# Performance work log

Hardware: AMD Instinct MI355X
Metric: run time of the kernel (lower is better)

## Reference

```python
import jax, jax.numpy as jnp
import numpy as np

B, NPER, K, H = 256, 512, 8, 16  # events, particles/event, knn k, hidden_dim
N = B * NPER


def _edge_conv(h, Wc, bc):
    """DynamicEdgeConv: per-event kNN graph, edge MLP on [x_i, x_j-x_i], max-aggregate."""
    d = h.shape[-1]
    hb = h.reshape(B, NPER, d)
    sq = jnp.sum(hb * hb, axis=-1)                                   # [B,n]
    d2 = sq[:, :, None] + sq[:, None, :] - 2.0 * jnp.einsum('bnd,bmd->bnm', hb, hb)
    _, idx = jax.lax.top_k(-d2, K)                                   # [B,n,K] nearest (incl. self)
    xj = jax.vmap(lambda hh, ii: hh[ii])(hb, idx)                    # [B,n,K,d] gather
    xi = jnp.broadcast_to(hb[:, :, None, :], xj.shape)               # [B,n,K,d]
    e = jnp.concatenate([xi, xj - xi], axis=-1)                      # [B,n,K,2d]
    m = jax.nn.elu(e @ Wc + bc)                                      # [B,n,K,H]
    return jnp.max(m, axis=2).reshape(N, -1)                         # scatter-max over neighbors


def setup_inputs() -> dict:
    key = jax.random.key(0)
    ks = jax.random.split(key, 10)
    def lin(k, fin, fout):
        return jax.random.normal(k, (fin, fout), jnp.float32) / np.sqrt(fin)
    x_pf = jax.random.normal(ks[0], (N, 4), jnp.float32)
    batch_pf = jnp.repeat(jnp.arange(B, dtype=jnp.int64), NPER)
    return {
        'x_pf': x_pf, 'batch_pf': batch_pf,
        'W1': lin(ks[1], 4, H),  'b1': jnp.zeros((H,), jnp.float32),
        'W2': lin(ks[2], H, H),  'b2': jnp.zeros((H,), jnp.float32),
        'Wc': lin(ks[3], 2 * H, H), 'bc': jnp.zeros((H,), jnp.float32),
        'Wo1': lin(ks[4], H, 8), 'bo1': jnp.zeros((8,), jnp.float32),
        'Wo2': lin(ks[5], 8, 4), 'bo2': jnp.zeros((4,), jnp.float32),
        'Wo3': lin(ks[6], 4, 1), 'bo3': jnp.zeros((1,), jnp.float32),
    }


def reference(x_pf, batch_pf, W1, b1, W2, b2, Wc, bc, Wo1, bo1, Wo2, bo2, Wo3, bo3):
    # pf_encode: Linear-ELU-Linear-ELU (assumes contiguous equal-size events per batch_pf)
    h = jax.nn.elu(x_pf @ W1 + b1)
    h = jax.nn.elu(h @ W2 + b2)                                      # [N,H]
    # two DynamicEdgeConv passes with SHARED weights (same self.conv called twice)
    f1 = _edge_conv(h, Wc, bc)
    f2 = _edge_conv(f1, Wc, bc)
    # avg_pool_x with cluster == batch -> per-event mean
    pooled = f2.reshape(B, NPER, -1).mean(axis=1)                    # [B,H]
    o = jax.nn.elu(pooled @ Wo1 + bo1)
    o = jax.nn.elu(o @ Wo2 + bo2)
    out = o @ Wo3 + bo3                                              # [B,1]
    return out, jnp.arange(B)
```

## Files before the change

### kernel.cpp

```cpp
#include <hip/hip_runtime.h>

#define NEV 256
#define NP  512
#define HD  16
#define GPAD 20
#define KBS 36

typedef short s16x8  __attribute__((ext_vector_type(8)));
typedef float f32x16 __attribute__((ext_vector_type(16)));

#define Z16 {0.f,0.f,0.f,0.f,0.f,0.f,0.f,0.f,0.f,0.f,0.f,0.f,0.f,0.f,0.f,0.f}

__device__ __forceinline__ float elu_f(float x) {
    return x > 0.0f ? x : (__expf(x) - 1.0f);
}
__device__ __forceinline__ unsigned umin_(unsigned a, unsigned b) { return a < b ? a : b; }
__device__ __forceinline__ unsigned med3u(unsigned a, unsigned b, unsigned c) {
    unsigned d;
    asm("v_med3_u32 %0, %1, %2, %3" : "=v"(d) : "v"(a), "v"(b), "v"(c));
    return d;
}
__device__ __forceinline__ unsigned short rneb(float f) {
    unsigned u = __float_as_uint(f);
    return (unsigned short)((u + 0x7FFFu + ((u >> 16) & 1u)) >> 16);
}
__device__ __forceinline__ float bits2f(unsigned short b) {
    return __uint_as_float(((unsigned)b) << 16);
}

__global__ __launch_bounds__(512) void suep_fused(
    const float* __restrict__ x_pf,
    const float* __restrict__ W1,  const float* __restrict__ b1,
    const float* __restrict__ W2,  const float* __restrict__ b2,
    const float* __restrict__ Wc,  const float* __restrict__ bc,
    const float* __restrict__ Wo1, const float* __restrict__ bo1,
    const float* __restrict__ Wo2, const float* __restrict__ bo2,
    const float* __restrict__ Wo3, const float* __restrict__ bo3,
    float* __restrict__ out)
{
    __shared__ unsigned kb[NP * KBS];
    __shared__ s16x8 fragH[16][64];
    __shared__ s16x8 fragL[16][64];
    __shared__ float sSq[NP];
    __shared__ float sW1[64],  sB1[HD];
    __shared__ float sW2[256], sB2[HD];
    __shared__ float sWcB[256], sWcD[256], sBc[HD];
    __shared__ float sWo1[128], sBo1[8], sWo2[32], sBo2[4], sWo3[4], sBo3[1];
    __shared__ float sRedM[8];
    __shared__ float sRed[8][HD];
    __shared__ float sPool[HD];

    const int tid   = threadIdx.x;
    const int ev    = blockIdx.x;
    const int l     = tid & 63;
    const int w     = tid >> 6;
    const int c32   = l & 31;
    const int khalf = l >> 5;

    if (tid < 64) sW1[tid] = W1[tid];
    if (tid < HD) { sB1[tid] = b1[tid]; sB2[tid] = b2[tid]; sBc[tid] = bc[tid]; }
    if (tid < 256) {
        sW2[tid] = W2[tid];
        float wb = Wc[256 + tid];
        sWcB[tid] = wb;
        sWcD[tid] = Wc[tid] - wb;
    }
    if (tid < 128) sWo1[tid] = Wo1[tid];
    if (tid < 8)   sBo1[tid] = bo1[tid];
    if (tid < 32)  sWo2[tid] = Wo2[tid];
    if (tid < 4)   { sBo2[tid] = bo2[tid]; sWo3[tid] = Wo3[tid]; }
    if (tid == 0)  sBo3[0] = bo3[0];
    __syncthreads();

    float4 xv = ((const float4*)x_pf)[ev * NP + tid];
    float e1[HD];
#pragma unroll
    for (int c = 0; c < HD; ++c) {
        float a = sB1[c];
        a = fmaf(xv.x, sW1[0 * HD + c], a);
        a = fmaf(xv.y, sW1[1 * HD + c], a);
        a = fmaf(xv.z, sW1[2 * HD + c], a);
        a = fmaf(xv.w, sW1[3 * HD + c], a);
        e1[c] = elu_f(a);
    }
    float h[HD];
#pragma unroll
    for (int c = 0; c < HD; ++c) {
        float a = sB2[c];
#pragma unroll
        for (int f = 0; f < HD; ++f) a = fmaf(e1[f], sW2[f * HD + c], a);
        h[c] = elu_f(a);
    }

    auto build_frags = [&](const float* hr) -> float {
        s16x8 vh0, vh1, vl0, vl1;
        float sq = 0.0f;
#pragma unroll
        for (int k = 0; k < HD; ++k) {
            unsigned short hb = rneb(hr[k]);
            float fh = bits2f(hb);
            float rr = hr[k] - fh;
            unsigned short lb = rneb(rr);
            float fl = bits2f(lb);
            float ht = fh + fl;
            sq = fmaf(ht, ht, sq);
            if (k < 8) { vh0[k] = (short)hb; vl0[k] = (short)lb; }
            else       { vh1[k - 8] = (short)hb; vl1[k - 8] = (short)lb; }
        }
        int b = tid >> 5, r = tid & 31;
        fragH[b][r]      = vh0;
        fragH[b][r + 32] = vh1;
        fragL[b][r]      = vl0;
        fragL[b][r + 32] = vl1;
        sSq[tid] = sq;
        float m = sq;
#pragma unroll
        for (int d = 32; d >= 1; d >>= 1) m = fmaxf(m, __shfl_xor(m, d, 64));
        if (l == 0) sRedM[w] = m;
        __syncthreads();
        float mx = sRedM[0];
#pragma unroll
        for (int i = 1; i < 8; ++i) mx = fmaxf(mx, sRedM[i]);
        return mx + 1.0f;
    };

    auto do_conv = [&](const float* hr, float* fout) {
        float Cv = build_frags(hr);

        s16x8 Ah0 = fragH[2 * w][l],     Al0 = fragL[2 * w][l];
        s16x8 Ah1 = fragH[2 * w + 1][l], Al1 = fragL[2 * w + 1][l];

        unsigned t0 = ~0u, t1 = ~0u, t2 = ~0u, t3 = ~0u,
                 t4 = ~0u, t5 = ~0u, t6 = ~0u, t7 = ~0u;
#define INS(KEY) do { unsigned kk = (KEY);            \
        t7 = med3u(t6, kk, t7); t6 = med3u(t5, kk, t6); \
        t5 = med3u(t4, kk, t5); t4 = med3u(t3, kk, t4); \
        t3 = med3u(t2, kk, t3); t2 = med3u(t1, kk, t2); \
        t1 = med3u(t0, kk, t1); t0 = umin_(kk, t0); } while (0)

        auto cs = [&](int s, f32x16& a0, f32x16& a1) {
            s16x8 Bh = fragH[s][l], Bl = fragL[s][l];
            f32x16 z = Z16;
            a0 = __builtin_amdgcn_mfma_f32_32x32x16_bf16(Al0, Bh, z,  0, 0, 0);
            a0 = __builtin_amdgcn_mfma_f32_32x32x16_bf16(Ah0, Bl, a0, 0, 0, 0);
            a0 = __builtin_amdgcn_mfma_f32_32x32x16_bf16(Ah0, Bh, a0, 0, 0, 0);
            a1 = __builtin_amdgcn_mfma_f32_32x32x16_bf16(Al1, Bh, z,  0, 0, 0);
            a1 = __builtin_amdgcn_mfma_f32_32x32x16_bf16(Ah1, Bl, a1, 0, 0, 0);
            a1 = __builtin_amdgcn_mfma_f32_32x32x16_bf16(Ah1, Bh, a1, 0, 0, 0);
        };

        unsigned* wp = &kb[(64 * w + 4 * khalf) * KBS + c32];
        auto st = [&](int s, const f32x16& a0, const f32x16& a1) {
            float base = Cv + sSq[s * 32 + c32];
            unsigned colb = (unsigned)(s * 32 + c32);
#pragma unroll
            for (int q = 0; q < 16; ++q) {
                const int roff = (q & 3) + 8 * (q >> 2);
                wp[roff * KBS] =
                    (__float_as_uint(fmaf(-2.0f, a0[q], base)) & 0xFFFFFE00u) | colb;
                wp[(32 + roff) * KBS] =
                    (__float_as_uint(fmaf(-2.0f, a1[q], base)) & 0xFFFFFE00u) | colb;
            }
        };

        const uint4* rp = (const uint4*)&kb[tid * KBS];
        auto scan = [&]() {
#pragma unroll
            for (int g = 0; g < 8; ++g) {
                uint4 k4 = rp[g];
                INS(k4.x); INS(k4.y); INS(k4.z); INS(k4.w);
            }
        };

        f32x16 aA, aB, nA, nB;
        cs(0, aA, aB);
        for (int s = 0; s < 16; s += 2) {
            st(s, aA, aB);
            cs(s + 1, nA, nB);
            asm volatile("s_waitcnt lgkmcnt(0)" ::: "memory");
            scan();
            st(s + 1, nA, nB);
            if (s + 2 < 16) cs(s + 2, aA, aB);
            asm volatile("s_waitcnt lgkmcnt(0)" ::: "memory");
            scan();
        }
#undef INS

        float gg[HD], bb[HD];
#pragma unroll
        for (int c = 0; c < HD; ++c) { gg[c] = 0.0f; bb[c] = sBc[c]; }
#pragma unroll
        for (int f = 0; f < HD; ++f) {
            float hf = hr[f];
#pragma unroll
            for (int c = 0; c < HD; ++c) {
                gg[c] = fmaf(hf, sWcB[f * HD + c], gg[c]);
                bb[c] = fmaf(hf, sWcD[f * HD + c], bb[c]);
            }
        }
        __syncthreads();
        float (*sG)[GPAD] = reinterpret_cast<float(*)[GPAD]>(kb);
        ((float4*)(&sG[tid][0]))[0] = make_float4(gg[0], gg[1], gg[2], gg[3]);
        ((float4*)(&sG[tid][0]))[1] = make_float4(gg[4], gg[5], gg[6], gg[7]);
        ((float4*)(&sG[tid][0]))[2] = make_float4(gg[8], gg[9], gg[10], gg[11]);
        ((float4*)(&sG[tid][0]))[3] = make_float4(gg[12], gg[13], gg[14], gg[15]);
        __syncthreads();

        int idx[8] = { (int)(t0 & 511u), (int)(t1 & 511u), (int)(t2 & 511u),
                       (int)(t3 & 511u), (int)(t4 & 511u), (int)(t5 & 511u),
                       (int)(t6 & 511u), (int)(t7 & 511u) };
        float z[HD];
#pragma unroll
        for (int c = 0; c < HD; ++c) z[c] = -3.4e38f;
#pragma unroll
        for (int n = 0; n < 8; ++n) {
            const float4* r4 = (const float4*)(&sG[idx[n]][0]);
            float4 va = r4[0], vb = r4[1], vc = r4[2], vd = r4[3];
            z[0]  = fmaxf(z[0],  bb[0]  + va.x);
            z[1]  = fmaxf(z[1],  bb[1]  + va.y);
            z[2]  = fmaxf(z[2],  bb[2]  + va.z);
            z[3]  = fmaxf(z[3],  bb[3]  + va.w);
            z[4]  = fmaxf(z[4],  bb[4]  + vb.x);
            z[5]  = fmaxf(z[5],  bb[5]  + vb.y);
            z[6]  = fmaxf(z[6],  bb[6]  + vb.z);
            z[7]  = fmaxf(z[7],  bb[7]  + vb.w);
            z[8]  = fmaxf(z[8],  bb[8]  + vc.x);
            z[9]  = fmaxf(z[9],  bb[9]  + vc.y);
            z[10] = fmaxf(z[10], bb[10] + vc.z);
            z[11] = fmaxf(z[11], bb[11] + vc.w);
            z[12] = fmaxf(z[12], bb[12] + vd.x);
            z[13] = fmaxf(z[13], bb[13] + vd.y);
            z[14] = fmaxf(z[14], bb[14] + vd.z);
            z[15] = fmaxf(z[15], bb[15] + vd.w);
        }
#pragma unroll
        for (int c = 0; c < HD; ++c) fout[c] = elu_f(z[c]);
    };

    float f1[HD], f2[HD];
    do_conv(h, f1);
    do_conv(f1, f2);

#pragma unroll
    for (int m = 32; m >= 1; m >>= 1) {
#pragma unroll
        for (int c = 0; c < HD; ++c) f2[c] += __shfl_xor(f2[c], m, 64);
    }
    if (l == 0) {
        ((float4*)(&sRed[w][0]))[0] = make_float4(f2[0], f2[1], f2[2], f2[3]);
        ((float4*)(&sRed[w][0]))[1] = make_float4(f2[4], f2[5], f2[6], f2[7]);
        ((float4*)(&sRed[w][0]))[2] = make_float4(f2[8], f2[9], f2[10], f2[11]);
        ((float4*)(&sRed[w][0]))[3] = make_float4(f2[12], f2[13], f2[14], f2[15]);
    }
    __syncthreads();
    if (tid < HD) {
        float s = 0.0f;
#pragma unroll
        for (int ww = 0; ww < 8; ++ww) s += sRed[ww][tid];
        sPool[tid] = s * (1.0f / (float)NP);
    }
    __syncthreads();

    if (tid == 0) {
        float o1[8];
#pragma unroll
        for (int c = 0; c < 8; ++c) {
            float a = sBo1[c];
#pragma unroll
            for (int f = 0; f < HD; ++f) a = fmaf(sPool[f], sWo1[f * 8 + c], a);
            o1[c] = elu_f(a);
        }
        float o2[4];
#pragma unroll
        for (int c = 0; c < 4; ++c) {
            float a = sBo2[c];
#pragma unroll
            for (int f = 0; f < 8; ++f) a = fmaf(o1[f], sWo2[f * 4 + c], a);
            o2[c] = elu_f(a);
        }
        float o3 = sBo3[0];
#pragma unroll
        for (int f = 0; f < 4; ++f) o3 = fmaf(o2[f], sWo3[f], o3);
        out[ev] = o3;
        out[NEV + ev] = (float)ev;
    }
}

extern "C" void kernel_launch(void* const* d_in, const int* in_sizes, int n_in,
                              void* d_out, int out_size, void* d_ws, size_t ws_size,
                              hipStream_t stream) {
    const float* x_pf = (const float*)d_in[0];
    const float* W1  = (const float*)d_in[2];
    const float* b1  = (const float*)d_in[3];
    const float* W2  = (const float*)d_in[4];
    const float* b2  = (const float*)d_in[5];
    const float* Wc  = (const float*)d_in[6];
    const float* bc  = (const float*)d_in[7];
    const float* Wo1 = (const float*)d_in[8];
    const float* bo1 = (const float*)d_in[9];
    const float* Wo2 = (const float*)d_in[10];
    const float* bo2 = (const float*)d_in[11];
    const float* Wo3 = (const float*)d_in[12];
    const float* bo3 = (const float*)d_in[13];
    float* out = (float*)d_out;

    hipLaunchKernelGGL(suep_fused, dim3(NEV), dim3(512), 0, stream,
                       x_pf, W1, b1, W2, b2, Wc, bc,
                       Wo1, bo1, Wo2, bo2, Wo3, bo3, out);
}
```

Before: 143.2 us.

## Split per-event work across 1024 threads with half-row kNN scans and merge

Doubles the block to 1024 threads, so each wave handles 32 query rows instead of 64. The two 32-lane halves scan separate halves of each key tile, and their sorted top-8 lists are merged with cross-lane shuffles. Fragment building, the edge-MLP precompute (the gather term in one half and the bias term in the other) and the neighbor max-gather are also split across the two thread halves, with conv outputs passed through shared memory. The aim is more waves per CU, with less per-thread register pressure and serial scan latency. The cost is extra barriers, shuffles and shared-memory round trips.

```diff
diff --git a/kernel.cpp b/kernel.cpp
--- a/kernel.cpp
+++ b/kernel.cpp
@@ -3,7 +3,6 @@
 #define NEV 256
 #define NP  512
 #define HD  16
-#define GPAD 20
 #define KBS 36
 
 typedef short s16x8  __attribute__((ext_vector_type(8)));
@@ -27,8 +26,11 @@
 __device__ __forceinline__ float bits2f(unsigned short b) {
     return __uint_as_float(((unsigned)b) << 16);
 }
-
-__global__ __launch_bounds__(512) void suep_fused(
+__device__ __forceinline__ unsigned sx32(unsigned v) {
+    return (unsigned)__shfl_xor((int)v, 32, 64);
+}
+
+__global__ __launch_bounds__(1024, 4) void suep_fused(
     const float* __restrict__ x_pf,
     const float* __restrict__ W1,  const float* __restrict__ b1,
     const float* __restrict__ W2,  const float* __restrict__ b2,
@@ -42,20 +44,19 @@
     __shared__ s16x8 fragH[16][64];
     __shared__ s16x8 fragL[16][64];
     __shared__ float sSq[NP];
-    __shared__ float sW1[64],  sB1[HD];
-    __shared__ float sW2[256], sB2[HD];
+    __shared__ float sW1[64], sB1[HD], sW2[256], sB2[HD];
     __shared__ float sWcB[256], sWcD[256], sBc[HD];
     __shared__ float sWo1[128], sBo1[8], sWo2[32], sBo2[4], sWo3[4], sBo3[1];
     __shared__ float sRedM[8];
-    __shared__ float sRed[8][HD];
+    __shared__ float sRed[16][HD];
     __shared__ float sPool[HD];
 
-    const int tid   = threadIdx.x;
-    const int ev    = blockIdx.x;
-    const int l     = tid & 63;
-    const int w     = tid >> 6;
-    const int c32   = l & 31;
-    const int khalf = l >> 5;
+    const int tid = threadIdx.x, ev = blockIdx.x;
+    const int l = tid & 63, w = tid >> 6;
+    const int n = tid & 511;
+    const bool loT = (tid < 512);
+    const int c32 = l & 31, kh = l >> 5;
+    const int row = 32 * w + c32;
 
     if (tid < 64) sW1[tid] = W1[tid];
     if (tid < HD) { sB1[tid] = b1[tid]; sB2[tid] = b2[tid]; sBc[tid] = bc[tid]; }
@@ -72,51 +73,53 @@
     if (tid == 0)  sBo3[0] = bo3[0];
     __syncthreads();
 
-    float4 xv = ((const float4*)x_pf)[ev * NP + tid];
-    float e1[HD];
-#pragma unroll
-    for (int c = 0; c < HD; ++c) {
-        float a = sB1[c];
-        a = fmaf(xv.x, sW1[0 * HD + c], a);
-        a = fmaf(xv.y, sW1[1 * HD + c], a);
-        a = fmaf(xv.z, sW1[2 * HD + c], a);
-        a = fmaf(xv.w, sW1[3 * HD + c], a);
-        e1[c] = elu_f(a);
+    float hr[HD];
+    {
+        float4 xv = ((const float4*)x_pf)[ev * NP + n];
+        float e1[HD];
+#pragma unroll
+        for (int c = 0; c < HD; ++c) {
+            float a = sB1[c];
+            a = fmaf(xv.x, sW1[0 * HD + c], a);
+            a = fmaf(xv.y, sW1[1 * HD + c], a);
+            a = fmaf(xv.z, sW1[2 * HD + c], a);
+            a = fmaf(xv.w, sW1[3 * HD + c], a);
+            e1[c] = elu_f(a);
+        }
+#pragma unroll
+        for (int c = 0; c < HD; ++c) {
+            float a = sB2[c];
+#pragma unroll
+            for (int f = 0; f < HD; ++f) a = fmaf(e1[f], sW2[f * HD + c], a);
+            hr[c] = elu_f(a);
+        }
     }
-    float h[HD];
-#pragma unroll
-    for (int c = 0; c < HD; ++c) {
-        float a = sB2[c];
-#pragma unroll
-        for (int f = 0; f < HD; ++f) a = fmaf(e1[f], sW2[f * HD + c], a);
-        h[c] = elu_f(a);
-    }
-
-    auto build_frags = [&](const float* hr) -> float {
-        s16x8 vh0, vh1, vl0, vl1;
+
+    auto build_frags = [&]() -> float {
+        s16x8 v0, v1;
         float sq = 0.0f;
 #pragma unroll
         for (int k = 0; k < HD; ++k) {
             unsigned short hb = rneb(hr[k]);
             float fh = bits2f(hb);
-            float rr = hr[k] - fh;
-            unsigned short lb = rneb(rr);
-            float fl = bits2f(lb);
-            float ht = fh + fl;
-            sq = fmaf(ht, ht, sq);
-            if (k < 8) { vh0[k] = (short)hb; vl0[k] = (short)lb; }
-            else       { vh1[k - 8] = (short)hb; vl1[k - 8] = (short)lb; }
-        }
-        int b = tid >> 5, r = tid & 31;
-        fragH[b][r]      = vh0;
-        fragH[b][r + 32] = vh1;
-        fragL[b][r]      = vl0;
-        fragL[b][r + 32] = vl1;
-        sSq[tid] = sq;
-        float m = sq;
-#pragma unroll
-        for (int d = 32; d >= 1; d >>= 1) m = fmaxf(m, __shfl_xor(m, d, 64));
-        if (l == 0) sRedM[w] = m;
+            unsigned short lb = rneb(hr[k] - fh);
+            if (loT) {
+                float ht = fh + bits2f(lb);
+                sq = fmaf(ht, ht, sq);
+            }
+            unsigned short vb = loT ? hb : lb;
+            if (k < 8) v0[k] = (short)vb; else v1[k - 8] = (short)vb;
+        }
+        s16x8 (*fr)[64] = loT ? fragH : fragL;
+        fr[n >> 5][n & 31]      = v0;
+        fr[n >> 5][(n & 31) + 32] = v1;
+        if (loT) {
+            sSq[n] = sq;
+            float m = sq;
+#pragma unroll
+            for (int d = 32; d >= 1; d >>= 1) m = fmaxf(m, __shfl_xor(m, d, 64));
+            if (l == 0) sRedM[w] = m;
+        }
         __syncthreads();
         float mx = sRedM[0];
 #pragma unroll
@@ -124,142 +127,161 @@
         return mx + 1.0f;
     };
 
-    auto do_conv = [&](const float* hr, float* fout) {
-        float Cv = build_frags(hr);
-
-        s16x8 Ah0 = fragH[2 * w][l],     Al0 = fragL[2 * w][l];
-        s16x8 Ah1 = fragH[2 * w + 1][l], Al1 = fragL[2 * w + 1][l];
+    auto do_conv = [&](bool last) {
+        float Cv = build_frags();
+
+        s16x8 Ah = fragH[w][l], Al = fragL[w][l];
 
         unsigned t0 = ~0u, t1 = ~0u, t2 = ~0u, t3 = ~0u,
                  t4 = ~0u, t5 = ~0u, t6 = ~0u, t7 = ~0u;
-#define INS(KEY) do { unsigned kk = (KEY);            \
+#define INS(KEY) do { unsigned kk = (KEY);              \
         t7 = med3u(t6, kk, t7); t6 = med3u(t5, kk, t6); \
         t5 = med3u(t4, kk, t5); t4 = med3u(t3, kk, t4); \
         t3 = med3u(t2, kk, t3); t2 = med3u(t1, kk, t2); \
         t1 = med3u(t0, kk, t1); t0 = umin_(kk, t0); } while (0)
 
-        auto cs = [&](int s, f32x16& a0, f32x16& a1) {
+        auto cs = [&](int s, f32x16& a) {
             s16x8 Bh = fragH[s][l], Bl = fragL[s][l];
             f32x16 z = Z16;
-            a0 = __builtin_amdgcn_mfma_f32_32x32x16_bf16(Al0, Bh, z,  0, 0, 0);
-            a0 = __builtin_amdgcn_mfma_f32_32x32x16_bf16(Ah0, Bl, a0, 0, 0, 0);
-            a0 = __builtin_amdgcn_mfma_f32_32x32x16_bf16(Ah0, Bh, a0, 0, 0, 0);
-            a1 = __builtin_amdgcn_mfma_f32_32x32x16_bf16(Al1, Bh, z,  0, 0, 0);
-            a1 = __builtin_amdgcn_mfma_f32_32x32x16_bf16(Ah1, Bl, a1, 0, 0, 0);
-            a1 = __builtin_amdgcn_mfma_f32_32x32x16_bf16(Ah1, Bh, a1, 0, 0, 0);
+            a = __builtin_amdgcn_mfma_f32_32x32x16_bf16(Al, Bh, z, 0, 0, 0);
+            a = __builtin_amdgcn_mfma_f32_32x32x16_bf16(Ah, Bl, a, 0, 0, 0);
+            a = __builtin_amdgcn_mfma_f32_32x32x16_bf16(Ah, Bh, a, 0, 0, 0);
         };
 
-        unsigned* wp = &kb[(64 * w + 4 * khalf) * KBS + c32];
-        auto st = [&](int s, const f32x16& a0, const f32x16& a1) {
-            float base = Cv + sSq[s * 32 + c32];
-            unsigned colb = (unsigned)(s * 32 + c32);
+        unsigned* wp = &kb[(32 * w + 4 * kh) * KBS + c32];
+        auto st = [&](int s, const f32x16& a) {
+            float base = Cv + sSq[32 * s + c32];
+            unsigned colb = (unsigned)(32 * s + c32);
 #pragma unroll
             for (int q = 0; q < 16; ++q) {
                 const int roff = (q & 3) + 8 * (q >> 2);
                 wp[roff * KBS] =
-                    (__float_as_uint(fmaf(-2.0f, a0[q], base)) & 0xFFFFFE00u) | colb;
-                wp[(32 + roff) * KBS] =
-                    (__float_as_uint(fmaf(-2.0f, a1[q], base)) & 0xFFFFFE00u) | colb;
+                    (__float_as_uint(fmaf(-2.0f, a[q], base)) & 0xFFFFFE00u) | colb;
             }
         };
 
-        const uint4* rp = (const uint4*)&kb[tid * KBS];
+        const uint4* rp = (const uint4*)&kb[row * KBS + 16 * kh];
         auto scan = [&]() {
 #pragma unroll
-            for (int g = 0; g < 8; ++g) {
+            for (int g = 0; g < 4; ++g) {
                 uint4 k4 = rp[g];
                 INS(k4.x); INS(k4.y); INS(k4.z); INS(k4.w);
             }
         };
 
-        f32x16 aA, aB, nA, nB;
-        cs(0, aA, aB);
+        f32x16 a0, a1;
+        cs(0, a0);
         for (int s = 0; s < 16; s += 2) {
-            st(s, aA, aB);
-            cs(s + 1, nA, nB);
+            st(s, a0);
+            cs(s + 1, a1);
             asm volatile("s_waitcnt lgkmcnt(0)" ::: "memory");
             scan();
-            st(s + 1, nA, nB);
-            if (s + 2 < 16) cs(s + 2, aA, aB);
+            st(s + 1, a1);
+            if (s + 2 < 16) cs(s + 2, a0);
             asm volatile("s_waitcnt lgkmcnt(0)" ::: "memory");
             scan();
         }
 #undef INS
 
-        float gg[HD], bb[HD];
-#pragma unroll
-        for (int c = 0; c < HD; ++c) { gg[c] = 0.0f; bb[c] = sBc[c]; }
-#pragma unroll
-        for (int f = 0; f < HD; ++f) {
-            float hf = hr[f];
-#pragma unroll
-            for (int c = 0; c < HD; ++c) {
-                gg[c] = fmaf(hf, sWcB[f * HD + c], gg[c]);
-                bb[c] = fmaf(hf, sWcD[f * HD + c], bb[c]);
+        unsigned m0 = umin_(t0, sx32(t7)), m1 = umin_(t1, sx32(t6)),
+                 m2 = umin_(t2, sx32(t5)), m3 = umin_(t3, sx32(t4)),
+                 m4 = umin_(t4, sx32(t3)), m5 = umin_(t5, sx32(t2)),
+                 m6 = umin_(t6, sx32(t1)), m7 = umin_(t7, sx32(t0));
+
+        float gb[HD];
+        {
+            const float* Wm = loT ? sWcB : sWcD;
+#pragma unroll
+            for (int c = 0; c < HD; ++c) gb[c] = loT ? 0.0f : sBc[c];
+#pragma unroll
+            for (int f = 0; f < HD; ++f) {
+                float hf = hr[f];
+#pragma unroll
+                for (int c = 0; c < HD; ++c) gb[c] = fmaf(hf, Wm[f * HD + c], gb[c]);
             }
         }
         __syncthreads();
-        float (*sG)[GPAD] = reinterpret_cast<float(*)[GPAD]>(kb);
-        ((float4*)(&sG[tid][0]))[0] = make_float4(gg[0], gg[1], gg[2], gg[3]);
-        ((float4*)(&sG[tid][0]))[1] = make_float4(gg[4], gg[5], gg[6], gg[7]);
-        ((float4*)(&sG[tid][0]))[2] = make_float4(gg[8], gg[9], gg[10], gg[11]);
-        ((float4*)(&sG[tid][0]))[3] = make_float4(gg[12], gg[13], gg[14], gg[15]);
+        float* gr = (float*)&kb[n * KBS + (loT ? 0 : 16)];
+        ((float4*)gr)[0] = make_float4(gb[0], gb[1], gb[2], gb[3]);
+        ((float4*)gr)[1] = make_float4(gb[4], gb[5], gb[6], gb[7]);
+        ((float4*)gr)[2] = make_float4(gb[8], gb[9], gb[10], gb[11]);
+        ((float4*)gr)[3] = make_float4(gb[12], gb[13], gb[14], gb[15]);
         __syncthreads();
 
-        int idx[8] = { (int)(t0 & 511u), (int)(t1 & 511u), (int)(t2 & 511u),
-                       (int)(t3 & 511u), (int)(t4 & 511u), (int)(t5 & 511u),
-                       (int)(t6 & 511u), (int)(t7 & 511u) };
+        int j0 = (int)((kh ? m4 : m0) & 511u), j1 = (int)((kh ? m5 : m1) & 511u);
+        int j2 = (int)((kh ? m6 : m2) & 511u), j3 = (int)((kh ? m7 : m3) & 511u);
         float z[HD];
-#pragma unroll
-        for (int c = 0; c < HD; ++c) z[c] = -3.4e38f;
-#pragma unroll
-        for (int n = 0; n < 8; ++n) {
-            const float4* r4 = (const float4*)(&sG[idx[n]][0]);
-            float4 va = r4[0], vb = r4[1], vc = r4[2], vd = r4[3];
-            z[0]  = fmaxf(z[0],  bb[0]  + va.x);
-            z[1]  = fmaxf(z[1],  bb[1]  + va.y);
-            z[2]  = fmaxf(z[2],  bb[2]  + va.z);
-            z[3]  = fmaxf(z[3],  bb[3]  + va.w);
-            z[4]  = fmaxf(z[4],  bb[4]  + vb.x);
-            z[5]  = fmaxf(z[5],  bb[5]  + vb.y);
-            z[6]  = fmaxf(z[6],  bb[6]  + vb.z);
-            z[7]  = fmaxf(z[7],  bb[7]  + vb.w);
-            z[8]  = fmaxf(z[8],  bb[8]  + vc.x);
-            z[9]  = fmaxf(z[9],  bb[9]  + vc.y);
-            z[10] = fmaxf(z[10], bb[10] + vc.z);
-            z[11] = fmaxf(z[11], bb[11] + vc.w);
-            z[12] = fmaxf(z[12], bb[12] + vd.x);
-            z[13] = fmaxf(z[13], bb[13] + vd.y);
-            z[14] = fmaxf(z[14], bb[14] + vd.z);
-            z[15] = fmaxf(z[15], bb[15] + vd.w);
-        }
-#pragma unroll
-        for (int c = 0; c < HD; ++c) fout[c] = elu_f(z[c]);
+        {
+            const float4* g0 = (const float4*)&kb[j0 * KBS];
+            const float4* g1 = (const float4*)&kb[j1 * KBS];
+            const float4* g2 = (const float4*)&kb[j2 * KBS];
+            const float4* g3 = (const float4*)&kb[j3 * KBS];
+#pragma unroll
+            for (int qq = 0; qq < 4; ++qq) {
+                float4 va = g0[qq], vb = g1[qq], vc = g2[qq], vd = g3[qq];
+                z[4*qq+0] = fmaxf(fmaxf(va.x, vb.x), fmaxf(vc.x, vd.x));
+                z[4*qq+1] = fmaxf(fmaxf(va.y, vb.y), fmaxf(vc.y, vd.y));
+                z[4*qq+2] = fmaxf(fmaxf(va.z, vb.z), fmaxf(vc.z, vd.z));
+                z[4*qq+3] = fmaxf(fmaxf(va.w, vb.w), fmaxf(vc.w, vd.w));
+            }
+        }
+#pragma unroll
+        for (int c = 0; c < HD; ++c) z[c] = fmaxf(z[c], __shfl_xor(z[c], 32, 64));
+
+        float fo[HD];
+        if (kh == 0) {
+            const float4* br = (const float4*)&kb[row * KBS + 16];
+#pragma unroll
+            for (int qq = 0; qq < 4; ++qq) {
+                float4 vb = br[qq];
+                fo[4*qq+0] = elu_f(z[4*qq+0] + vb.x);
+                fo[4*qq+1] = elu_f(z[4*qq+1] + vb.y);
+                fo[4*qq+2] = elu_f(z[4*qq+2] + vb.z);
+                fo[4*qq+3] = elu_f(z[4*qq+3] + vb.w);
+            }
+        }
+
+        if (!last) {
+            __syncthreads();
+            if (kh == 0) {
+                float4* fr = (float4*)&kb[row * KBS];
+                fr[0] = make_float4(fo[0], fo[1], fo[2], fo[3]);
+                fr[1] = make_float4(fo[4], fo[5], fo[6], fo[7]);
+                fr[2] = make_float4(fo[8], fo[9], fo[10], fo[11]);
+                fr[3] = make_float4(fo[12], fo[13], fo[14], fo[15]);
+            }
+            __syncthreads();
+            const float4* hrp = (const float4*)&kb[n * KBS];
+#pragma unroll
+            for (int qq = 0; qq < 4; ++qq) {
+                float4 v = hrp[qq];
+                hr[4*qq+0] = v.x; hr[4*qq+1] = v.y; hr[4*qq+2] = v.z; hr[4*qq+3] = v.w;
+            }
+        } else {
+#pragma unroll
+            for (int m = 16; m >= 1; m >>= 1) {
+#pragma unroll
+                for (int c = 0; c < HD; ++c) fo[c] += __shfl_xor(fo[c], m, 64);
+            }
+            if (l == 0) {
+                ((float4*)(&sRed[w][0]))[0] = make_float4(fo[0], fo[1], fo[2], fo[3]);
+                ((float4*)(&sRed[w][0]))[1] = make_float4(fo[4], fo[5], fo[6], fo[7]);
+                ((float4*)(&sRed[w][0]))[2] = make_float4(fo[8], fo[9], fo[10], fo[11]);
+                ((float4*)(&sRed[w][0]))[3] = make_float4(fo[12], fo[13], fo[14], fo[15]);
+            }
+            __syncthreads();
+            if (tid < HD) {
+                float s = 0.0f;
+#pragma unroll
+                for (int ww = 0; ww < 16; ++ww) s += sRed[ww][tid];
+                sPool[tid] = s * (1.0f / (float)NP);
+            }
+            __syncthreads();
+        }
     };
 
-    float f1[HD], f2[HD];
-    do_conv(h, f1);
-    do_conv(f1, f2);
-
-#pragma unroll
-    for (int m = 32; m >= 1; m >>= 1) {
-#pragma unroll
-        for (int c = 0; c < HD; ++c) f2[c] += __shfl_xor(f2[c], m, 64);
-    }
-    if (l == 0) {
-        ((float4*)(&sRed[w][0]))[0] = make_float4(f2[0], f2[1], f2[2], f2[3]);
-        ((float4*)(&sRed[w][0]))[1] = make_float4(f2[4], f2[5], f2[6], f2[7]);
-        ((float4*)(&sRed[w][0]))[2] = make_float4(f2[8], f2[9], f2[10], f2[11]);
-        ((float4*)(&sRed[w][0]))[3] = make_float4(f2[12], f2[13], f2[14], f2[15]);
-    }
-    __syncthreads();
-    if (tid < HD) {
-        float s = 0.0f;
-#pragma unroll
-        for (int ww = 0; ww < 8; ++ww) s += sRed[ww][tid];
-        sPool[tid] = s * (1.0f / (float)NP);
-    }
-    __syncthreads();
+    do_conv(false);
+    do_conv(true);
 
     if (tid == 0) {
         float o1[8];
@@ -304,7 +326,7 @@
     const float* bo3 = (const float*)d_in[13];
     float* out = (float*)d_out;
 
-    hipLaunchKernelGGL(suep_fused, dim3(NEV), dim3(512), 0, stream,
+    hipLaunchKernelGGL(suep_fused, dim3(NEV), dim3(1024), 0, stream,
                        x_pf, W1, b1, W2, b2, Wc, bc,
                        Wo1, bo1, Wo2, bo2, Wo3, bo3, out);
 }
```

Result: no change. 145.8 us (+1.8%).
